# Kernel optimization log

Hardware: AMD Instinct MI355X
Metric: run time of the kernel (lower is better)

Reference implementation:

```python
import jax, jax.numpy as jnp
import numpy as np

N_NODES = 100000
N_EDGES = 1600000
IN_DIM = 128
HID_DIM = 128
OUT_DIM = 64


def gcn_conv(x, W, b, edge_index):
    """GCNConv with add_self_loops, symmetric degree norm, add-aggregation.

    Math matches PyG: out[i] = sum_{(j,i) in E+selfloops} norm_ji * (x_j @ W) + b
    Since lin is linear and there is no edge_attr, we transform x once before
    the gather instead of per-edge (identical result, far less FLOPs/traffic).
    """
    n = x.shape[0]
    loop = jnp.arange(n, dtype=edge_index.dtype)
    row = jnp.concatenate([edge_index[0], loop])  # source nodes (x_j)
    col = jnp.concatenate([edge_index[1], loop])  # destination nodes
    # degree over destinations (includes self loops -> deg >= 1, no div by 0)
    deg = jax.ops.segment_sum(jnp.ones_like(col, dtype=x.dtype), col, num_segments=n)
    dinv = jax.lax.rsqrt(deg)
    norm = dinv[row] * dinv[col]  # [E+N]
    h = x @ W  # [N, out] transform once
    msg = norm[:, None] * h[row]  # [E+N, out] gathered per-edge messages
    out = jax.ops.segment_sum(msg, col, num_segments=n)  # scatter-add
    return out + b


def setup_inputs() -> dict:
    key = jax.random.key(0)
    k1, k2, k3, k4 = jax.random.split(key, 4)
    x = jax.random.normal(k1, (N_NODES, IN_DIM), dtype=jnp.float32)
    edge_index = jax.random.randint(k2, (2, N_EDGES), 0, N_NODES, dtype=jnp.int64)
    # glorot-ish init
    W1 = jax.random.normal(k3, (IN_DIM, HID_DIM), dtype=jnp.float32) * (2.0 / (IN_DIM + HID_DIM)) ** 0.5
    W2 = jax.random.normal(k4, (HID_DIM, OUT_DIM), dtype=jnp.float32) * (2.0 / (HID_DIM + OUT_DIM)) ** 0.5
    b1 = jnp.zeros((HID_DIM,), dtype=jnp.float32)
    b2 = jnp.zeros((OUT_DIM,), dtype=jnp.float32)
    return {"x": x, "edge_index": edge_index, "W1": W1, "b1": b1, "W2": W2, "b2": b2}


def reference(x, edge_index, W1, b1, W2, b2):
    # GCN.forward with prompt_type=None, pooling=False, eval mode (dropout is identity)
    h = gcn_conv(x, W1, b1, edge_index)
    h = jax.nn.relu(h)
    out = gcn_conv(h, W2, b2, edge_index)
    return out
```

## Files before the change

kernel.cpp:

```cpp
#include <hip/hip_runtime.h>


#define DIN 128
#define DHID 128
#define DOUT 64
#define ELLW 64
#define GPART 8
#define BPG 512

typedef __attribute__((ext_vector_type(4))) float f32x4;
typedef __attribute__((ext_vector_type(8))) short bf16x8;

__device__ __forceinline__ float bf2f(unsigned int u16) {
    return __uint_as_float(u16 << 16);
}
__device__ __forceinline__ unsigned short f2bf(float f) {
    unsigned int u = __float_as_uint(f);
    u += 0x7fffu + ((u >> 16) & 1u);
    return (unsigned short)(u >> 16);
}
__device__ __forceinline__ unsigned int pack2(float a, float b) {
    return (unsigned int)f2bf(a) | ((unsigned int)f2bf(b) << 16);
}

__global__ __launch_bounds__(256) void k_packW(const float* __restrict__ W1,
                                               const float* __restrict__ W2,
                                               unsigned short* __restrict__ w1p,
                                               unsigned short* __restrict__ w2p,
                                               int* __restrict__ deg, int N) {
    int id = blockIdx.x * 256 + threadIdx.x;
    if (id < 2048) {
        int lane = id & 63, s = (id >> 6) & 3, t = id >> 8;
        int n = t * 16 + (lane & 15);
        int k0 = s * 32 + (lane >> 4) * 8;
#pragma unroll
        for (int j = 0; j < 8; ++j)
            w1p[(size_t)id * 8 + j] = f2bf(W1[(k0 + j) * DHID + n]);
    } else if (id < 3072) {
        int id2 = id - 2048;
        int lane = id2 & 63, s = (id2 >> 6) & 3, t = id2 >> 8;
        int n = t * 16 + (lane & 15);
        int k0 = s * 32 + (lane >> 4) * 8;
#pragma unroll
        for (int j = 0; j < 8; ++j)
            w2p[(size_t)id2 * 8 + j] = f2bf(W2[(k0 + j) * DOUT + n]);
    }
    for (int i = id; i < N; i += 12 * 256) deg[i] = 0;
}

__device__ __forceinline__ void fill_edge(int c, int r, int lo, int hi,
                                          int* __restrict__ deg, int* __restrict__ ell) {
    if (c >= lo && c < hi) {
        int k = atomicAdd(&deg[c], 1);
        if (k < ELLW) ell[(size_t)c * ELLW + k] = r;
    }
}

__global__ __launch_bounds__(256) void k_fill_gemm1(
        const int* __restrict__ rows, const int* __restrict__ cols,
        int* __restrict__ deg, int* __restrict__ ell,
        int E, int perBlock, int R, int GOCT, int GB,
        const float* __restrict__ x, const unsigned short* __restrict__ w1p,
        unsigned short* __restrict__ h1b, int N) {
    int bid = (int)blockIdx.x;
    int o = bid >> 3;
    int lane7 = bid & 7;
    int m = o / 3;
    int p = o - 3 * m;
    if (p == 2 && m < GOCT) {
        int gemmIdx = m * 8 + lane7;
        if (gemmIdx >= GB) return;
        int wave = threadIdx.x >> 6, lane = threadIdx.x & 63;
        int quad = lane >> 4, qr = lane & 15;
        int rowBase = gemmIdx * 64 + wave * 16;
        int arow = rowBase + qr;
        bool rowOK = arow < N;
        f32x4 acc[8] = {};
#pragma unroll
        for (int s = 0; s < 4; ++s) {
            bf16x8 a = {};
            if (rowOK) {
                const float* ap = x + (size_t)arow * DIN + s * 32 + quad * 8;
                float4 lo = *(const float4*)ap;
                float4 hi = *(const float4*)(ap + 4);
                a[0] = (short)f2bf(lo.x); a[1] = (short)f2bf(lo.y);
                a[2] = (short)f2bf(lo.z); a[3] = (short)f2bf(lo.w);
                a[4] = (short)f2bf(hi.x); a[5] = (short)f2bf(hi.y);
                a[6] = (short)f2bf(hi.z); a[7] = (short)f2bf(hi.w);
            }
#pragma unroll
            for (int t = 0; t < 8; ++t) {
                bf16x8 b = *(const bf16x8*)(w1p + ((size_t)(t * 4 + s) * 64 + lane) * 8);
                acc[t] = __builtin_amdgcn_mfma_f32_16x16x32_bf16(a, b, acc[t], 0, 0, 0);
            }
        }
#pragma unroll
        for (int t = 0; t < 8; ++t)
#pragma unroll
            for (int i = 0; i < 4; ++i) {
                int r = rowBase + quad * 4 + i;
                if (r < N) h1b[(size_t)r * DHID + t * 16 + qr] = f2bf(acc[t][i]);
            }
        return;
    }
    int gemBefore = (m < GOCT) ? m : GOCT;
    int chunk = o - gemBefore;
    int g = lane7;
    int lo = g * R, hi = lo + R;
    int eBeg = chunk * perBlock;
    int eEnd = eBeg + perBlock; if (eEnd > E) eEnd = E;
    for (int e = eBeg + 4 * threadIdx.x; e < eEnd; e += 4 * 256) {
        if (e + 3 < eEnd) {
            int4 c4 = *(const int4*)(cols + e);
            int4 r4 = *(const int4*)(rows + e);
            fill_edge(c4.x, r4.x, lo, hi, deg, ell);
            fill_edge(c4.y, r4.y, lo, hi, deg, ell);
            fill_edge(c4.z, r4.z, lo, hi, deg, ell);
            fill_edge(c4.w, r4.w, lo, hi, deg, ell);
        } else {
            for (int j = e; j < eEnd; ++j) fill_edge(cols[j], rows[j], lo, hi, deg, ell);
        }
    }
}

__global__ __launch_bounds__(256) void k_gather1g2(const int* __restrict__ deg,
                                                   const int* __restrict__ ell,
                                                   const uint2* __restrict__ h1v,
                                                   const float* __restrict__ b1,
                                                   const unsigned short* __restrict__ w2p,
                                                   unsigned short* __restrict__ h2b, int N) {
    __shared__ unsigned short hact_s[16][136];
    int wv = threadIdx.x >> 6;
    int lane = threadIdx.x & 63;
    int half = lane >> 5, col = lane & 31;
    int base = blockIdx.x * 16;
    float4 bv = *(const float4*)(b1 + 4 * col);
    for (int i = 0; i < 4; ++i) {
        int w = base + wv * 4 + i;
        if (w < N) {
            int d = deg[w]; if (d > ELLW) d = ELLW;
            int iv = 0;
            if (lane < d) iv = ell[(size_t)w * ELLW + lane];
            float dv = (lane < d) ? rsqrtf((float)(deg[iv] + 1)) : 0.f;
            float a0 = 0.f, a1 = 0.f, a2 = 0.f, a3 = 0.f;
            int e = 0;
            for (; e + 16 <= d; e += 16) {
                int s[8]; float wg[8]; uint2 v[8];
#pragma unroll
                for (int j = 0; j < 8; ++j) {
                    int idx = e + 2 * j + half;
                    s[j] = __shfl(iv, idx); wg[j] = __shfl(dv, idx);
                }
#pragma unroll
                for (int j = 0; j < 8; ++j) v[j] = h1v[(size_t)s[j] * 32 + col];
#pragma unroll
                for (int j = 0; j < 8; ++j) {
                    a0 = fmaf(wg[j], bf2f(v[j].x & 0xffffu), a0);
                    a1 = fmaf(wg[j], bf2f(v[j].x >> 16), a1);
                    a2 = fmaf(wg[j], bf2f(v[j].y & 0xffffu), a2);
                    a3 = fmaf(wg[j], bf2f(v[j].y >> 16), a3);
                }
            }
            if (e + 8 <= d) {
                int s[4]; float wg[4]; uint2 v[4];
#pragma unroll
                for (int j = 0; j < 4; ++j) {
                    int idx = e + 2 * j + half;
                    s[j] = __shfl(iv, idx); wg[j] = __shfl(dv, idx);
                }
#pragma unroll
                for (int j = 0; j < 4; ++j) v[j] = h1v[(size_t)s[j] * 32 + col];
#pragma unroll
                for (int j = 0; j < 4; ++j) {
                    a0 = fmaf(wg[j], bf2f(v[j].x & 0xffffu), a0);
                    a1 = fmaf(wg[j], bf2f(v[j].x >> 16), a1);
                    a2 = fmaf(wg[j], bf2f(v[j].y & 0xffffu), a2);
                    a3 = fmaf(wg[j], bf2f(v[j].y >> 16), a3);
                }
                e += 8;
            }
            if (e < d) {
                int s[4]; float wg[4]; uint2 v[4];
#pragma unroll
                for (int j = 0; j < 4; ++j) {
                    int idx = e + 2 * j + half;
                    int cl = idx < 63 ? idx : 63;
                    s[j] = __shfl(iv, cl);
                    float t = __shfl(dv, cl);
                    wg[j] = (idx < d) ? t : 0.f;
                }
#pragma unroll
                for (int j = 0; j < 4; ++j) v[j] = h1v[(size_t)s[j] * 32 + col];
#pragma unroll
                for (int j = 0; j < 4; ++j) {
                    a0 = fmaf(wg[j], bf2f(v[j].x & 0xffffu), a0);
                    a1 = fmaf(wg[j], bf2f(v[j].x >> 16), a1);
                    a2 = fmaf(wg[j], bf2f(v[j].y & 0xffffu), a2);
                    a3 = fmaf(wg[j], bf2f(v[j].y >> 16), a3);
                }
            }
            a0 += __shfl_xor(a0, 32); a1 += __shfl_xor(a1, 32);
            a2 += __shfl_xor(a2, 32); a3 += __shfl_xor(a3, 32);
            float di = rsqrtf((float)(d + 1)), self = di * di;
            uint2 hv = h1v[(size_t)w * 32 + col];
            float r0 = fmaf(di, a0, fmaf(self, bf2f(hv.x & 0xffffu), bv.x));
            float r1 = fmaf(di, a1, fmaf(self, bf2f(hv.x >> 16), bv.y));
            float r2 = fmaf(di, a2, fmaf(self, bf2f(hv.y & 0xffffu), bv.z));
            float r3 = fmaf(di, a3, fmaf(self, bf2f(hv.y >> 16), bv.w));
            if (lane < 32) {
                uint2 ov;
                ov.x = pack2(fmaxf(r0, 0.f), fmaxf(r1, 0.f));
                ov.y = pack2(fmaxf(r2, 0.f), fmaxf(r3, 0.f));
                *(uint2*)&hact_s[wv * 4 + i][4 * col] = ov;
            }
        } else if (lane < 32) {
            uint2 z; z.x = 0u; z.y = 0u;
            *(uint2*)&hact_s[wv * 4 + i][4 * col] = z;
        }
    }
    __syncthreads();
    int quad = lane >> 4, qr = lane & 15;
    f32x4 acc = {};
#pragma unroll
    for (int s = 0; s < 4; ++s) {
        bf16x8 a = *(const bf16x8*)&hact_s[qr][s * 32 + quad * 8];
        bf16x8 b = *(const bf16x8*)(w2p + ((size_t)(wv * 4 + s) * 64 + lane) * 8);
        acc = __builtin_amdgcn_mfma_f32_16x16x32_bf16(a, b, acc, 0, 0, 0);
    }
#pragma unroll
    for (int i = 0; i < 4; ++i) {
        int r = base + quad * 4 + i;
        if (r < N) h2b[(size_t)r * DOUT + wv * 16 + qr] = f2bf(acc[i]);
    }
}

__global__ __launch_bounds__(256) void k_gather2(const int* __restrict__ deg,
                                                 const int* __restrict__ ell,
                                                 const unsigned int* __restrict__ h2v,
                                                 const float* __restrict__ b2,
                                                 float* __restrict__ out, int N) {
    int w = (blockIdx.x * 256 + threadIdx.x) >> 6;
    int lane = threadIdx.x & 63;
    if (w >= N) return;
    int d = deg[w]; if (d > ELLW) d = ELLW;
    int iv = 0;
    if (lane < d) iv = ell[(size_t)w * ELLW + lane];
    float dv = (lane < d) ? rsqrtf((float)(deg[iv] + 1)) : 0.f;
    int half = lane >> 5, col = lane & 31;
    float a0 = 0.f, a1 = 0.f;
    int e = 0;
    for (; e + 16 <= d; e += 16) {
        int s[8]; float wg[8]; unsigned int v[8];
#pragma unroll
        for (int j = 0; j < 8; ++j) {
            int idx = e + 2 * j + half;
            s[j] = __shfl(iv, idx); wg[j] = __shfl(dv, idx);
        }
#pragma unroll
        for (int j = 0; j < 8; ++j) v[j] = h2v[(size_t)s[j] * 32 + col];
#pragma unroll
        for (int j = 0; j < 8; ++j) {
            a0 = fmaf(wg[j], bf2f(v[j] & 0xffffu), a0);
            a1 = fmaf(wg[j], bf2f(v[j] >> 16), a1);
        }
    }
    if (e + 8 <= d) {
        int s[4]; float wg[4]; unsigned int v[4];
#pragma unroll
        for (int j = 0; j < 4; ++j) {
            int idx = e + 2 * j + half;
            s[j] = __shfl(iv, idx); wg[j] = __shfl(dv, idx);
        }
#pragma unroll
        for (int j = 0; j < 4; ++j) v[j] = h2v[(size_t)s[j] * 32 + col];
#pragma unroll
        for (int j = 0; j < 4; ++j) {
            a0 = fmaf(wg[j], bf2f(v[j] & 0xffffu), a0);
            a1 = fmaf(wg[j], bf2f(v[j] >> 16), a1);
        }
        e += 8;
    }
    if (e < d) {
        int s[4]; float wg[4]; unsigned int v[4];
#pragma unroll
        for (int j = 0; j < 4; ++j) {
            int idx = e + 2 * j + half;
            int cl = idx < 63 ? idx : 63;
            s[j] = __shfl(iv, cl);
            float t = __shfl(dv, cl);
            wg[j] = (idx < d) ? t : 0.f;
        }
#pragma unroll
        for (int j = 0; j < 4; ++j) v[j] = h2v[(size_t)s[j] * 32 + col];
#pragma unroll
        for (int j = 0; j < 4; ++j) {
            a0 = fmaf(wg[j], bf2f(v[j] & 0xffffu), a0);
            a1 = fmaf(wg[j], bf2f(v[j] >> 16), a1);
        }
    }
    a0 += __shfl_xor(a0, 32); a1 += __shfl_xor(a1, 32);
    float di = rsqrtf((float)(d + 1)), self = di * di;
    unsigned int hv = h2v[(size_t)w * 32 + col];
    float2 bv = *(const float2*)(b2 + 2 * col);
    float r0 = fmaf(di, a0, fmaf(self, bf2f(hv & 0xffffu), bv.x));
    float r1 = fmaf(di, a1, fmaf(self, bf2f(hv >> 16), bv.y));
    if (lane < 32) {
        float2 ov; ov.x = r0; ov.y = r1;
        *(float2*)(out + (size_t)w * DOUT + 2 * col) = ov;
    }
}

extern "C" void kernel_launch(void* const* d_in, const int* in_sizes, int n_in,
                              void* d_out, int out_size, void* d_ws, size_t ws_size,
                              hipStream_t stream) {
    const float* x  = (const float*)d_in[0];
    const int*   ei = (const int*)d_in[1];
    const float* W1 = (const float*)d_in[2];
    const float* b1 = (const float*)d_in[3];
    const float* W2 = (const float*)d_in[4];
    const float* b2 = (const float*)d_in[5];

    const int N = in_sizes[0] / DIN;
    const int E = in_sizes[1] / 2;
    const int* rows = ei;
    const int* cols = ei + E;

    char* p = (char*)d_ws;
    int*   ell  = (int*)p;                    p += (size_t)N * ELLW * 4;
    unsigned short* h1b = (unsigned short*)p;   p += (size_t)N * DHID * 2;
    unsigned short* h2b = (unsigned short*)p;   p += (size_t)N * DOUT * 2;
    unsigned short* w1p = (unsigned short*)p;   p += (size_t)2048 * 8 * 2;
    unsigned short* w2p = (unsigned short*)p;   p += (size_t)1024 * 8 * 2;
    int*   deg  = (int*)p;                    p += (size_t)N * 4;

    const int R = (N + GPART - 1) / GPART;
    int perBlock = (E + BPG - 1) / BPG;
    perBlock = (perBlock + 3) & ~3;
    const int GB = (N + 63) / 64;
    const int GOCT = (GB + 7) / 8;
    const int OCT = BPG + GOCT;

    k_packW<<<12, 256, 0, stream>>>(W1, W2, w1p, w2p, deg, N);

    k_fill_gemm1<<<8 * OCT, 256, 0, stream>>>(rows, cols, deg, ell, E, perBlock, R,
                                              GOCT, GB, x, w1p, h1b, N);

    k_gather1g2<<<(N + 15) / 16, 256, 0, stream>>>(deg, ell, (const uint2*)h1b,
                                                   b1, w2p, h2b, N);

    k_gather2<<<(N + 3) / 4, 256, 0, stream>>>(deg, ell, (const unsigned int*)h2b,
                                               b2, (float*)d_out, N);
}
```

Before: 295.9 us.

## Assign fill-edge partitions by XCC ID with dynamic chunk cursors and workgroup-scope atomics

The edge-fill blocks now pick their destination-node partition from the hardware XCC ID instead of the block index. Each block then pulls edge chunks from a per-XCC atomic cursor until all chunks are done. The degree atomics are relaxed to workgroup scope, on the assumption that all updates to a partition stay within one XCC's L2, which avoids device-scope atomic cost and cross-die traffic. The risk is correctness: it depends on the hardware-to-XCC mapping being consistent and every XCC running at least one block. It also adds cursor atomics and two barriers per chunk.

```diff
diff --git a/kernel.cpp b/kernel.cpp
--- a/kernel.cpp
+++ b/kernel.cpp
@@ -7,6 +7,7 @@
 #define ELLW 64
 #define GPART 8
 #define BPG 512
+#define NCHUNK 512
 
 typedef __attribute__((ext_vector_type(4))) float f32x4;
 typedef __attribute__((ext_vector_type(8))) short bf16x8;
@@ -27,7 +28,8 @@
                                                const float* __restrict__ W2,
                                                unsigned short* __restrict__ w1p,
                                                unsigned short* __restrict__ w2p,
-                                               int* __restrict__ deg, int N) {
+                                               int* __restrict__ deg,
+                                               int* __restrict__ cursors, int N) {
     int id = blockIdx.x * 256 + threadIdx.x;
     if (id < 2048) {
         int lane = id & 63, s = (id >> 6) & 3, t = id >> 8;
@@ -45,21 +47,23 @@
         for (int j = 0; j < 8; ++j)
             w2p[(size_t)id2 * 8 + j] = f2bf(W2[(k0 + j) * DOUT + n]);
     }
+    if (id < 128) cursors[id] = 0;
     for (int i = id; i < N; i += 12 * 256) deg[i] = 0;
 }
 
 __device__ __forceinline__ void fill_edge(int c, int r, int lo, int hi,
                                           int* __restrict__ deg, int* __restrict__ ell) {
     if (c >= lo && c < hi) {
-        int k = atomicAdd(&deg[c], 1);
+        int k = __hip_atomic_fetch_add(&deg[c], 1, __ATOMIC_RELAXED,
+                                       __HIP_MEMORY_SCOPE_WORKGROUP);
         if (k < ELLW) ell[(size_t)c * ELLW + k] = r;
     }
 }
 
 __global__ __launch_bounds__(256) void k_fill_gemm1(
         const int* __restrict__ rows, const int* __restrict__ cols,
-        int* __restrict__ deg, int* __restrict__ ell,
-        int E, int perBlock, int R, int GOCT, int GB,
+        int* __restrict__ deg, int* __restrict__ ell, int* __restrict__ cursors,
+        int E, int perChunk, int R, int GOCT, int GB,
         const float* __restrict__ x, const unsigned short* __restrict__ w1p,
         unsigned short* __restrict__ h1b, int N) {
     int bid = (int)blockIdx.x;
@@ -103,22 +107,30 @@
             }
         return;
     }
-    int gemBefore = (m < GOCT) ? m : GOCT;
-    int chunk = o - gemBefore;
-    int g = lane7;
+    unsigned xcc;
+    asm volatile("s_getreg_b32 %0, hwreg(HW_REG_XCC_ID)" : "=s"(xcc));
+    int g = (int)(xcc & 7u);
     int lo = g * R, hi = lo + R;
-    int eBeg = chunk * perBlock;
-    int eEnd = eBeg + perBlock; if (eEnd > E) eEnd = E;
-    for (int e = eBeg + 4 * threadIdx.x; e < eEnd; e += 4 * 256) {
-        if (e + 3 < eEnd) {
-            int4 c4 = *(const int4*)(cols + e);
-            int4 r4 = *(const int4*)(rows + e);
-            fill_edge(c4.x, r4.x, lo, hi, deg, ell);
-            fill_edge(c4.y, r4.y, lo, hi, deg, ell);
-            fill_edge(c4.z, r4.z, lo, hi, deg, ell);
-            fill_edge(c4.w, r4.w, lo, hi, deg, ell);
-        } else {
-            for (int j = e; j < eEnd; ++j) fill_edge(cols[j], rows[j], lo, hi, deg, ell);
+    __shared__ int s_chunk;
+    for (;;) {
+        __syncthreads();
+        if (threadIdx.x == 0) s_chunk = atomicAdd(&cursors[g * 16], 1);
+        __syncthreads();
+        int chunk = s_chunk;
+        if (chunk >= NCHUNK) break;
+        int eBeg = chunk * perChunk;
+        int eEnd = eBeg + perChunk; if (eEnd > E) eEnd = E;
+        for (int e = eBeg + 4 * (int)threadIdx.x; e < eEnd; e += 4 * 256) {
+            if (e + 3 < eEnd) {
+                int4 c4 = *(const int4*)(cols + e);
+                int4 r4 = *(const int4*)(rows + e);
+                fill_edge(c4.x, r4.x, lo, hi, deg, ell);
+                fill_edge(c4.y, r4.y, lo, hi, deg, ell);
+                fill_edge(c4.z, r4.z, lo, hi, deg, ell);
+                fill_edge(c4.w, r4.w, lo, hi, deg, ell);
+            } else {
+                for (int j = e; j < eEnd; ++j) fill_edge(cols[j], rows[j], lo, hi, deg, ell);
+            }
         }
     }
 }
@@ -332,18 +344,20 @@
     unsigned short* w1p = (unsigned short*)p;   p += (size_t)2048 * 8 * 2;
     unsigned short* w2p = (unsigned short*)p;   p += (size_t)1024 * 8 * 2;
     int*   deg  = (int*)p;                    p += (size_t)N * 4;
+    int*   cursors = (int*)p;                 p += 128 * 4;
 
     const int R = (N + GPART - 1) / GPART;
-    int perBlock = (E + BPG - 1) / BPG;
-    perBlock = (perBlock + 3) & ~3;
+    int perChunk = (E + NCHUNK - 1) / NCHUNK;
+    perChunk = (perChunk + 3) & ~3;
     const int GB = (N + 63) / 64;
     const int GOCT = (GB + 7) / 8;
     const int OCT = BPG + GOCT;
 
-    k_packW<<<12, 256, 0, stream>>>(W1, W2, w1p, w2p, deg, N);
-
-    k_fill_gemm1<<<8 * OCT, 256, 0, stream>>>(rows, cols, deg, ell, E, perBlock, R,
-                                              GOCT, GB, x, w1p, h1b, N);
+    k_packW<<<12, 256, 0, stream>>>(W1, W2, w1p, w2p, deg, cursors, N);
+
+    k_fill_gemm1<<<8 * OCT, 256, 0, stream>>>(rows, cols, deg, ell, cursors,
+                                              E, perChunk, R, GOCT, GB,
+                                              x, w1p, h1b, N);
 
     k_gather1g2<<<(N + 15) / 16, 256, 0, stream>>>(deg, ell, (const uint2*)h1b,
                                                    b1, w2p, h2b, N);
```

Result: slower. 307.3 us (+3.9%).
